# Performance work log

Hardware: AMD Instinct MI355X
Metric: run time of the kernel (lower is better)

Reference implementation:

```python
import jax, jax.numpy as jnp
import numpy as np

N = 50000      # nodes
E = 500000     # edges (avg degree 10)
IN = 256       # in_feats
HID = 64       # hid_feats (per-head out dim)
H = 4          # num_heads


def setup_inputs() -> dict:
    key = jax.random.key(0)
    ks = jax.random.split(key, 16)
    f32 = jnp.float32
    def rn(k, shape, s=0.05):
        return jax.random.normal(k, shape, dtype=f32) * s
    return {
        "x": jax.random.normal(ks[0], (N, IN), dtype=f32),
        "src": jax.random.randint(ks[1], (E,), 0, N, dtype=jnp.int32),
        "dst": jax.random.randint(ks[2], (E,), 0, N, dtype=jnp.int32),
        "embed_W": rn(ks[3], (IN, HID)), "embed_b": jnp.zeros((HID,), f32),
        "W1": rn(ks[4], (HID, H * HID)),
        "al1": rn(ks[5], (H, HID)), "ar1": rn(ks[6], (H, HID)),
        "b1": jnp.zeros((H * HID,), f32),
        "W2": rn(ks[7], (H * HID, H * HID)),
        "al2": rn(ks[8], (H, HID)), "ar2": rn(ks[9], (H, HID)),
        "b2": jnp.zeros((H * HID,), f32),
        "p1_W": rn(ks[10], (H * HID, HID)), "p1_b": jnp.zeros((HID,), f32),
        "p2_W": rn(ks[11], (HID, 1)), "p2_b": jnp.zeros((1,), f32),
    }


def _gat_conv(x, W, al, ar, b, src, dst):
    """DGL GATConv: linear proj, per-edge LeakyReLU attention, edge softmax over dst, scatter-sum."""
    feat = (x @ W).reshape(N, H, HID)                    # [N,H,F]
    el = jnp.einsum('nhf,hf->nh', feat, al)              # [N,H]
    er = jnp.einsum('nhf,hf->nh', feat, ar)              # [N,H]
    e = jax.nn.leaky_relu(el[src] + er[dst], 0.2)        # [E,H]
    m = jax.ops.segment_max(e, dst, num_segments=N)      # per-dst max (stable softmax)
    ex = jnp.exp(e - m[dst])                             # [E,H]
    s = jax.ops.segment_sum(ex, dst, num_segments=N)     # [N,H]
    alpha = ex / s[dst]                                  # edge softmax weights
    out = jax.ops.segment_sum(alpha[:, :, None] * feat[src], dst, num_segments=N)  # [N,H,F]
    return out + b.reshape(1, H, HID)


def reference(x, src, dst, embed_W, embed_b, W1, al1, ar1, b1,
              W2, al2, ar2, b2, p1_W, p1_b, p2_W, p2_b):
    h = x @ embed_W + embed_b                                        # embed: [N,HID]
    h = jax.nn.relu(_gat_conv(h, W1, al1, ar1, b1, src, dst))        # [N,H,HID]
    h = h.reshape(N, H * HID)
    h = jax.nn.relu(_gat_conv(h, W2, al2, ar2, b2, src, dst))        # [N,H,HID]
    h = h.reshape(N, H * HID)
    return jax.nn.sigmoid((h @ p1_W + p1_b) @ p2_W + p2_b)           # [N,1]
```

## Files before the change

### kernel.cpp

```cpp
#include <hip/hip_runtime.h>
#include <hip/hip_bf16.h>

#define NN 50000
#define NE 500000
#define C_HH 256

typedef __attribute__((ext_vector_type(8))) short s16x8;
typedef __attribute__((ext_vector_type(4))) float f32x4;
typedef __attribute__((ext_vector_type(4))) unsigned short u16x4;
typedef unsigned short ushort_t;

__device__ __forceinline__ float lrelu(float x) { return x > 0.f ? x : 0.2f * x; }

__device__ __forceinline__ ushort_t f2bf(float f) {
  unsigned u = __float_as_uint(f);
  u = (u + 0x7FFFu + ((u >> 16) & 1u)) >> 16;
  return (ushort_t)u;
}
__device__ __forceinline__ float bf2f(ushort_t u) {
  return __uint_as_float(((unsigned)u) << 16);
}
__device__ __forceinline__ float sel_head(float4 v, int head) {
  const float x0 = (head & 1) ? v.y : v.x;
  const float x1 = (head & 1) ? v.w : v.z;
  return (head & 2) ? x1 : x0;
}

__global__ __launch_bounds__(256) void prep_kernel(const float* __restrict__ eW,
                                                   const float* __restrict__ W1,
                                                   const float* __restrict__ eb,
                                                   const float* __restrict__ W2,
                                                   const float* __restrict__ p1W,
                                                   const float* __restrict__ p1b,
                                                   const float* __restrict__ p2W,
                                                   const float* __restrict__ p2b,
                                                   ushort_t* __restrict__ WcT,
                                                   ushort_t* __restrict__ w2T,
                                                   float* __restrict__ bc,
                                                   float* __restrict__ qv,
                                                   float* __restrict__ cv) {
  int idx = blockIdx.x * 256 + threadIdx.x;
  if (idx < 65536) {
    const int n = idx >> 8, k = idx & 255;
    float s = 0.f;
#pragma unroll 8
    for (int j = 0; j < 64; ++j) s = fmaf(eW[k * 64 + j], W1[j * 256 + n], s);
    WcT[idx] = f2bf(s);
  } else if (idx < 131072) {
    idx -= 65536;
    const int n = idx >> 8, k = idx & 255;
    w2T[idx] = f2bf(W2[k * 256 + n]);
  } else if (idx < 131328) {
    const int n = idx - 131072;
    float s = 0.f;
#pragma unroll 8
    for (int j = 0; j < 64; ++j) s = fmaf(eb[j], W1[j * 256 + n], s);
    bc[n] = s;
  } else if (idx < 131584) {
    const int k = idx - 131328;
    float s = 0.f;
#pragma unroll 8
    for (int j = 0; j < 64; ++j) s = fmaf(p1W[k * 64 + j], p2W[j], s);
    qv[k] = s;
  } else if (idx == 131584) {
    float s = p2b[0];
    for (int j = 0; j < 64; ++j) s = fmaf(p1b[j], p2W[j], s);
    cv[0] = s;
  }
}

template <bool A_F32, bool BIAS>
__global__ __launch_bounds__(256) void gemm_fused(const void* __restrict__ Ain,
                                                  const ushort_t* __restrict__ WT,
                                                  const float* __restrict__ bc,
                                                  const float* __restrict__ al,
                                                  const float* __restrict__ ar,
                                                  float* __restrict__ el,
                                                  float* __restrict__ er,
                                                  ushort_t* __restrict__ Cout, int M) {
  const int wid = threadIdx.x >> 6;
  const int lane = threadIdx.x & 63;
  const int row0 = blockIdx.x * 32;
  const int rA = lane & 15;
  const int kg = lane >> 4;
  const int c0 = wid * 64;

  f32x4 acc[2][4] = {};
  const s16x8 zf = {0, 0, 0, 0, 0, 0, 0, 0};
  const bool v0 = (row0 + rA) < M;
  const bool v1 = (row0 + 16 + rA) < M;
  const ushort_t* Wbase = WT + (size_t)(c0 + rA) * 256;

  for (int ks = 0; ks < 8; ++ks) {
    const int k0 = ks * 32 + kg * 8;
    s16x8 a0 = zf, a1 = zf;
    if (A_F32) {
      const float* Af = (const float*)Ain;
      if (v0) {
        const f32x4 u0 = *reinterpret_cast<const f32x4*>(Af + (size_t)(row0 + rA) * 256 + k0);
        const f32x4 u1 = *reinterpret_cast<const f32x4*>(Af + (size_t)(row0 + rA) * 256 + k0 + 4);
        a0[0] = (short)f2bf(u0[0]); a0[1] = (short)f2bf(u0[1]);
        a0[2] = (short)f2bf(u0[2]); a0[3] = (short)f2bf(u0[3]);
        a0[4] = (short)f2bf(u1[0]); a0[5] = (short)f2bf(u1[1]);
        a0[6] = (short)f2bf(u1[2]); a0[7] = (short)f2bf(u1[3]);
      }
      if (v1) {
        const f32x4 u0 = *reinterpret_cast<const f32x4*>(Af + (size_t)(row0 + 16 + rA) * 256 + k0);
        const f32x4 u1 = *reinterpret_cast<const f32x4*>(Af + (size_t)(row0 + 16 + rA) * 256 + k0 + 4);
        a1[0] = (short)f2bf(u0[0]); a1[1] = (short)f2bf(u0[1]);
        a1[2] = (short)f2bf(u0[2]); a1[3] = (short)f2bf(u0[3]);
        a1[4] = (short)f2bf(u1[0]); a1[5] = (short)f2bf(u1[1]);
        a1[6] = (short)f2bf(u1[2]); a1[7] = (short)f2bf(u1[3]);
      }
    } else {
      const ushort_t* Ab = (const ushort_t*)Ain;
      if (v0) a0 = *reinterpret_cast<const s16x8*>(Ab + (size_t)(row0 + rA) * 256 + k0);
      if (v1) a1 = *reinterpret_cast<const s16x8*>(Ab + (size_t)(row0 + 16 + rA) * 256 + k0);
    }
#pragma unroll
    for (int nt = 0; nt < 4; ++nt) {
      const s16x8 b = *reinterpret_cast<const s16x8*>(Wbase + nt * 16 * 256 + k0);
      acc[0][nt] = __builtin_amdgcn_mfma_f32_16x16x32_bf16(a0, b, acc[0][nt], 0, 0, 0);
      acc[1][nt] = __builtin_amdgcn_mfma_f32_16x16x32_bf16(a1, b, acc[1][nt], 0, 0, 0);
    }
  }

  if (BIAS) {
#pragma unroll
    for (int nt = 0; nt < 4; ++nt) {
      const float bv = bc[c0 + nt * 16 + rA];
#pragma unroll
      for (int mt = 0; mt < 2; ++mt)
#pragma unroll
        for (int i = 0; i < 4; ++i) acc[mt][nt][i] += bv;
    }
  }

#pragma unroll
  for (int nt = 0; nt < 4; ++nt) {
    const int col = c0 + nt * 16 + rA;
#pragma unroll
    for (int mt = 0; mt < 2; ++mt) {
#pragma unroll
      for (int i = 0; i < 4; ++i) {
        const int row = row0 + mt * 16 + kg * 4 + i;
        if (row < M) Cout[(size_t)row * 256 + col] = f2bf(acc[mt][nt][i]);
      }
    }
  }

  float alv[4], arv[4];
#pragma unroll
  for (int nt = 0; nt < 4; ++nt) {
    alv[nt] = al[c0 + nt * 16 + rA];
    arv[nt] = ar[c0 + nt * 16 + rA];
  }
#pragma unroll
  for (int mt = 0; mt < 2; ++mt) {
#pragma unroll
    for (int i = 0; i < 4; ++i) {
      float e = 0.f, r = 0.f;
#pragma unroll
      for (int nt = 0; nt < 4; ++nt) {
        e = fmaf(acc[mt][nt][i], alv[nt], e);
        r = fmaf(acc[mt][nt][i], arv[nt], r);
      }
#pragma unroll
      for (int m = 1; m < 16; m <<= 1) {
        e += __shfl_xor(e, m);
        r += __shfl_xor(r, m);
      }
      const int row = row0 + mt * 16 + kg * 4 + i;
      if (rA == 0 && row < M) {
        el[row * 4 + wid] = e;
        er[row * 4 + wid] = r;
      }
    }
  }
}

__global__ __launch_bounds__(256) void hist_kernel(const int* __restrict__ dst,
                                                   int* __restrict__ rowptr) {
  const int e = blockIdx.x * 256 + threadIdx.x;
  if (e < NE) atomicAdd(&rowptr[dst[e]], 1);
}

__global__ __launch_bounds__(256) void scan1_kernel(int* __restrict__ rowptr,
                                                    int* __restrict__ partial) {
  __shared__ int sh[256];
  const int t = threadIdx.x;
  const int i = blockIdx.x * 256 + t;
  const int v = (i < NN) ? rowptr[i] : 0;
  sh[t] = v;
  __syncthreads();
#pragma unroll
  for (int off = 1; off < 256; off <<= 1) {
    int x = (t >= off) ? sh[t - off] : 0;
    __syncthreads();
    sh[t] += x;
    __syncthreads();
  }
  if (i < NN) rowptr[i] = sh[t] - v;
  if (t == 255) partial[blockIdx.x] = sh[255];
}

__global__ __launch_bounds__(256) void scan2_kernel(int* __restrict__ partial, int npb) {
  __shared__ int sh[256];
  const int t = threadIdx.x;
  const int v = (t < npb) ? partial[t] : 0;
  sh[t] = v;
  __syncthreads();
#pragma unroll
  for (int off = 1; off < 256; off <<= 1) {
    int x = (t >= off) ? sh[t - off] : 0;
    __syncthreads();
    sh[t] += x;
    __syncthreads();
  }
  if (t < npb) partial[t] = sh[t] - v;
}

__global__ __launch_bounds__(256) void scan3_kernel(int* __restrict__ rowptr,
                                                    const int* __restrict__ partial,
                                                    int* __restrict__ cursor) {
  const int i = blockIdx.x * 256 + threadIdx.x;
  if (i < NN) {
    const int r = rowptr[i] + partial[i >> 8];
    rowptr[i] = r;
    cursor[i] = r;
  } else if (i == NN) {
    rowptr[NN] = NE;
  }
}

__global__ __launch_bounds__(256) void scatter_kernel(const int* __restrict__ src,
                                                      const int* __restrict__ dst,
                                                      int* __restrict__ cursor,
                                                      int* __restrict__ sorted_src) {
  const int e = blockIdx.x * 256 + threadIdx.x;
  if (e >= NE) return;
  const int pos = atomicAdd(&cursor[dst[e]], 1);
  sorted_src[pos] = src[e];
}

__global__ __launch_bounds__(256) void aggr_fused_kernel(const int* __restrict__ rowptr,
                                                         const int* __restrict__ sorted_src,
                                                         const float* __restrict__ el,
                                                         const float* __restrict__ er,
                                                         const ushort_t* __restrict__ featb,
                                                         const float* __restrict__ bias,
                                                         ushort_t* __restrict__ out) {
  const int node = blockIdx.x * 4 + (threadIdx.x >> 6);
  const int lane = threadIdx.x & 63;
  const int head = lane >> 4;
  const int start = rowptr[node];
  const int end = rowptr[node + 1];
  const float erh = sel_head(*reinterpret_cast<const float4*>(er + node * 4), head);
  const size_t lofs = (size_t)lane * 4;

  float a0 = 0.f, a1 = 0.f, a2 = 0.f, a3 = 0.f, s = 0.f;
  int e = start;
  const int end4 = end - 3;
  for (; e < end4; e += 4) {
    const int sn0 = sorted_src[e + 0];
    const int sn1 = sorted_src[e + 1];
    const int sn2 = sorted_src[e + 2];
    const int sn3 = sorted_src[e + 3];
    const float4 A0 = *reinterpret_cast<const float4*>(el + sn0 * 4);
    const float4 A1 = *reinterpret_cast<const float4*>(el + sn1 * 4);
    const float4 A2 = *reinterpret_cast<const float4*>(el + sn2 * 4);
    const float4 A3 = *reinterpret_cast<const float4*>(el + sn3 * 4);
    const u16x4 F0 = *reinterpret_cast<const u16x4*>(featb + (size_t)sn0 * C_HH + lofs);
    const u16x4 F1 = *reinterpret_cast<const u16x4*>(featb + (size_t)sn1 * C_HH + lofs);
    const u16x4 F2 = *reinterpret_cast<const u16x4*>(featb + (size_t)sn2 * C_HH + lofs);
    const u16x4 F3 = *reinterpret_cast<const u16x4*>(featb + (size_t)sn3 * C_HH + lofs);
    const float w0 = __expf(lrelu(sel_head(A0, head) + erh));
    const float w1 = __expf(lrelu(sel_head(A1, head) + erh));
    const float w2 = __expf(lrelu(sel_head(A2, head) + erh));
    const float w3 = __expf(lrelu(sel_head(A3, head) + erh));
    a0 = fmaf(w0, bf2f(F0[0]), a0); a1 = fmaf(w0, bf2f(F0[1]), a1);
    a2 = fmaf(w0, bf2f(F0[2]), a2); a3 = fmaf(w0, bf2f(F0[3]), a3);
    a0 = fmaf(w1, bf2f(F1[0]), a0); a1 = fmaf(w1, bf2f(F1[1]), a1);
    a2 = fmaf(w1, bf2f(F1[2]), a2); a3 = fmaf(w1, bf2f(F1[3]), a3);
    a0 = fmaf(w2, bf2f(F2[0]), a0); a1 = fmaf(w2, bf2f(F2[1]), a1);
    a2 = fmaf(w2, bf2f(F2[2]), a2); a3 = fmaf(w2, bf2f(F2[3]), a3);
    a0 = fmaf(w3, bf2f(F3[0]), a0); a1 = fmaf(w3, bf2f(F3[1]), a1);
    a2 = fmaf(w3, bf2f(F3[2]), a2); a3 = fmaf(w3, bf2f(F3[3]), a3);
    s += (w0 + w1) + (w2 + w3);
  }
  for (; e < end; ++e) {
    const int sn = sorted_src[e];
    const float4 A = *reinterpret_cast<const float4*>(el + sn * 4);
    const u16x4 F = *reinterpret_cast<const u16x4*>(featb + (size_t)sn * C_HH + lofs);
    const float w = __expf(lrelu(sel_head(A, head) + erh));
    a0 = fmaf(w, bf2f(F[0]), a0); a1 = fmaf(w, bf2f(F[1]), a1);
    a2 = fmaf(w, bf2f(F[2]), a2); a3 = fmaf(w, bf2f(F[3]), a3);
    s += w;
  }

  float r0 = 0.f, r1 = 0.f, r2 = 0.f, r3 = 0.f;
  if (end > start) {
    const float inv = 1.f / s;
    r0 = a0 * inv; r1 = a1 * inv; r2 = a2 * inv; r3 = a3 * inv;
  }
  const float4 bb = *reinterpret_cast<const float4*>(bias + lane * 4);
  u16x4 o;
  o[0] = f2bf(fmaxf(r0 + bb.x, 0.f));
  o[1] = f2bf(fmaxf(r1 + bb.y, 0.f));
  o[2] = f2bf(fmaxf(r2 + bb.z, 0.f));
  o[3] = f2bf(fmaxf(r3 + bb.w, 0.f));
  *reinterpret_cast<u16x4*>(out + (size_t)node * C_HH + lane * 4) = o;
}

__global__ __launch_bounds__(256) void head_kernel(const ushort_t* __restrict__ houtb,
                                                   const float* __restrict__ qv,
                                                   const float* __restrict__ cv,
                                                   float* __restrict__ out) {
  const int node = blockIdx.x * 4 + (threadIdx.x >> 6);
  const int lane = threadIdx.x & 63;
  const u16x4 f = *reinterpret_cast<const u16x4*>(houtb + (size_t)node * C_HH + lane * 4);
  const float4 q = *reinterpret_cast<const float4*>(qv + lane * 4);
  float v = bf2f(f[0]) * q.x + bf2f(f[1]) * q.y + bf2f(f[2]) * q.z + bf2f(f[3]) * q.w;
#pragma unroll
  for (int off = 32; off; off >>= 1) v += __shfl_xor(v, off);
  if (lane == 0) out[node] = 1.f / (1.f + __expf(-(v + cv[0])));
}

extern "C" void kernel_launch(void* const* d_in, const int* in_sizes, int n_in,
                              void* d_out, int out_size, void* d_ws, size_t ws_size,
                              hipStream_t stream) {
  const float* x = (const float*)d_in[0];
  const int* src = (const int*)d_in[1];
  const int* dst = (const int*)d_in[2];
  const float* embed_W = (const float*)d_in[3];
  const float* embed_b = (const float*)d_in[4];
  const float* W1 = (const float*)d_in[5];
  const float* al1 = (const float*)d_in[6];
  const float* ar1 = (const float*)d_in[7];
  const float* b1 = (const float*)d_in[8];
  const float* W2 = (const float*)d_in[9];
  const float* al2 = (const float*)d_in[10];
  const float* ar2 = (const float*)d_in[11];
  const float* b2 = (const float*)d_in[12];
  const float* p1_W = (const float*)d_in[13];
  const float* p1_b = (const float*)d_in[14];
  const float* p2_W = (const float*)d_in[15];
  const float* p2_b = (const float*)d_in[16];

  char* ws = (char*)d_ws;
  ushort_t* featb = (ushort_t*)(ws + 0);
  ushort_t* houtb = (ushort_t*)(ws + 25600000);
  float* el = (float*)(ws + 51200000);
  float* er = (float*)(ws + 52000000);
  int* rowptr = (int*)(ws + 52800000);
  int* cursor = (int*)(ws + 53100000);
  int* partial = (int*)(ws + 53400000);
  int* sorted_src = (int*)(ws + 53500000);
  ushort_t* WcT = (ushort_t*)(ws + 55600000);
  ushort_t* w2T = (ushort_t*)(ws + 55800000);
  float* bc = (float*)(ws + 56000000);
  float* qv = (float*)(ws + 56010000);
  float* cv = (float*)(ws + 56020000);

  const int gEdge = (NE + 255) / 256;
  const int nScanB = (NN + 255) / 256;
  const int gGemm = (NN + 31) / 32;
  const int gNode = NN / 4;

  hipMemsetAsync(rowptr, 0, (NN + 1) * sizeof(int), stream);
  hist_kernel<<<gEdge, 256, 0, stream>>>(dst, rowptr);
  scan1_kernel<<<nScanB, 256, 0, stream>>>(rowptr, partial);
  scan2_kernel<<<1, 256, 0, stream>>>(partial, nScanB);
  scan3_kernel<<<nScanB + 1, 256, 0, stream>>>(rowptr, partial, cursor);
  scatter_kernel<<<gEdge, 256, 0, stream>>>(src, dst, cursor, sorted_src);

  prep_kernel<<<515, 256, 0, stream>>>(embed_W, W1, embed_b, W2, p1_W, p1_b, p2_W, p2_b,
                                       WcT, w2T, bc, qv, cv);

  gemm_fused<true, true><<<gGemm, 256, 0, stream>>>(x, WcT, bc, al1, ar1, el, er, featb, NN);
  aggr_fused_kernel<<<gNode, 256, 0, stream>>>(rowptr, sorted_src, el, er, featb, b1, houtb);

  gemm_fused<false, false><<<gGemm, 256, 0, stream>>>(houtb, w2T, nullptr, al2, ar2, el, er, featb, NN);
  aggr_fused_kernel<<<gNode, 256, 0, stream>>>(rowptr, sorted_src, el, er, featb, b2, houtb);

  head_kernel<<<gNode, 256, 0, stream>>>(houtb, qv, cv, (float*)d_out);
}
```

Measured before the change: 379.2 us.

## Fuse output head into second aggregation, preload GEMM operands, unroll edges by 8

The second GAT aggregation now computes the projection-head dot product and sigmoid directly, instead of writing bf16 hidden features for a separate head kernel. That removes one launch and a full write and re-read of the node features. The GEMM now issues all A and B loads up front into registers before the MFMA loop, with launch bounds asking for 2 blocks per SM. This raises register pressure in exchange for more memory-level parallelism. The aggregation edge loop is unrolled to 8 gathers per iteration to keep more loads in flight.

```diff
diff --git a/kernel.cpp b/kernel.cpp
--- a/kernel.cpp
+++ b/kernel.cpp
@@ -70,14 +70,14 @@
 }
 
 template <bool A_F32, bool BIAS>
-__global__ __launch_bounds__(256) void gemm_fused(const void* __restrict__ Ain,
-                                                  const ushort_t* __restrict__ WT,
-                                                  const float* __restrict__ bc,
-                                                  const float* __restrict__ al,
-                                                  const float* __restrict__ ar,
-                                                  float* __restrict__ el,
-                                                  float* __restrict__ er,
-                                                  ushort_t* __restrict__ Cout, int M) {
+__global__ __launch_bounds__(256, 2) void gemm_fused(const void* __restrict__ Ain,
+                                                     const ushort_t* __restrict__ WT,
+                                                     const float* __restrict__ bc,
+                                                     const float* __restrict__ al,
+                                                     const float* __restrict__ ar,
+                                                     float* __restrict__ el,
+                                                     float* __restrict__ er,
+                                                     ushort_t* __restrict__ Cout, int M) {
   const int wid = threadIdx.x >> 6;
   const int lane = threadIdx.x & 63;
   const int row0 = blockIdx.x * 32;
@@ -85,43 +85,65 @@
   const int kg = lane >> 4;
   const int c0 = wid * 64;
 
-  f32x4 acc[2][4] = {};
   const s16x8 zf = {0, 0, 0, 0, 0, 0, 0, 0};
   const bool v0 = (row0 + rA) < M;
   const bool v1 = (row0 + 16 + rA) < M;
   const ushort_t* Wbase = WT + (size_t)(c0 + rA) * 256;
 
+  s16x8 a0[8], a1[8];
+  if (A_F32) {
+    const float* Af = (const float*)Ain;
+    const float* Ar0 = Af + (size_t)(row0 + rA) * 256;
+    const float* Ar1 = Af + (size_t)(row0 + 16 + rA) * 256;
+    const f32x4 zf4 = {0.f, 0.f, 0.f, 0.f};
+    f32x4 af0[8][2], af1[8][2];
+#pragma unroll
+    for (int ks = 0; ks < 8; ++ks) {
+      const int k0 = ks * 32 + kg * 8;
+      af0[ks][0] = v0 ? *reinterpret_cast<const f32x4*>(Ar0 + k0) : zf4;
+      af0[ks][1] = v0 ? *reinterpret_cast<const f32x4*>(Ar0 + k0 + 4) : zf4;
+      af1[ks][0] = v1 ? *reinterpret_cast<const f32x4*>(Ar1 + k0) : zf4;
+      af1[ks][1] = v1 ? *reinterpret_cast<const f32x4*>(Ar1 + k0 + 4) : zf4;
+    }
+#pragma unroll
+    for (int ks = 0; ks < 8; ++ks) {
+#pragma unroll
+      for (int h = 0; h < 2; ++h) {
+#pragma unroll
+        for (int j = 0; j < 4; ++j) {
+          a0[ks][h * 4 + j] = (short)f2bf(af0[ks][h][j]);
+          a1[ks][h * 4 + j] = (short)f2bf(af1[ks][h][j]);
+        }
+      }
+    }
+  } else {
+    const ushort_t* Ab = (const ushort_t*)Ain;
+    const ushort_t* Ar0 = Ab + (size_t)(row0 + rA) * 256;
+    const ushort_t* Ar1 = Ab + (size_t)(row0 + 16 + rA) * 256;
+#pragma unroll
+    for (int ks = 0; ks < 8; ++ks) {
+      const int k0 = ks * 32 + kg * 8;
+      a0[ks] = v0 ? *reinterpret_cast<const s16x8*>(Ar0 + k0) : zf;
+      a1[ks] = v1 ? *reinterpret_cast<const s16x8*>(Ar1 + k0) : zf;
+    }
+  }
+
+  s16x8 b[8][4];
+#pragma unroll
   for (int ks = 0; ks < 8; ++ks) {
     const int k0 = ks * 32 + kg * 8;
-    s16x8 a0 = zf, a1 = zf;
-    if (A_F32) {
-      const float* Af = (const float*)Ain;
-      if (v0) {
-        const f32x4 u0 = *reinterpret_cast<const f32x4*>(Af + (size_t)(row0 + rA) * 256 + k0);
-        const f32x4 u1 = *reinterpret_cast<const f32x4*>(Af + (size_t)(row0 + rA) * 256 + k0 + 4);
-        a0[0] = (short)f2bf(u0[0]); a0[1] = (short)f2bf(u0[1]);
-        a0[2] = (short)f2bf(u0[2]); a0[3] = (short)f2bf(u0[3]);
-        a0[4] = (short)f2bf(u1[0]); a0[5] = (short)f2bf(u1[1]);
-        a0[6] = (short)f2bf(u1[2]); a0[7] = (short)f2bf(u1[3]);
-      }
-      if (v1) {
-        const f32x4 u0 = *reinterpret_cast<const f32x4*>(Af + (size_t)(row0 + 16 + rA) * 256 + k0);
-        const f32x4 u1 = *reinterpret_cast<const f32x4*>(Af + (size_t)(row0 + 16 + rA) * 256 + k0 + 4);
-        a1[0] = (short)f2bf(u0[0]); a1[1] = (short)f2bf(u0[1]);
-        a1[2] = (short)f2bf(u0[2]); a1[3] = (short)f2bf(u0[3]);
-        a1[4] = (short)f2bf(u1[0]); a1[5] = (short)f2bf(u1[1]);
-        a1[6] = (short)f2bf(u1[2]); a1[7] = (short)f2bf(u1[3]);
-      }
-    } else {
-      const ushort_t* Ab = (const ushort_t*)Ain;
-      if (v0) a0 = *reinterpret_cast<const s16x8*>(Ab + (size_t)(row0 + rA) * 256 + k0);
-      if (v1) a1 = *reinterpret_cast<const s16x8*>(Ab + (size_t)(row0 + 16 + rA) * 256 + k0);
-    }
+#pragma unroll
+    for (int nt = 0; nt < 4; ++nt)
+      b[ks][nt] = *reinterpret_cast<const s16x8*>(Wbase + nt * 16 * 256 + k0);
+  }
+
+  f32x4 acc[2][4] = {};
+#pragma unroll
+  for (int ks = 0; ks < 8; ++ks) {
 #pragma unroll
     for (int nt = 0; nt < 4; ++nt) {
-      const s16x8 b = *reinterpret_cast<const s16x8*>(Wbase + nt * 16 * 256 + k0);
-      acc[0][nt] = __builtin_amdgcn_mfma_f32_16x16x32_bf16(a0, b, acc[0][nt], 0, 0, 0);
-      acc[1][nt] = __builtin_amdgcn_mfma_f32_16x16x32_bf16(a1, b, acc[1][nt], 0, 0, 0);
+      acc[0][nt] = __builtin_amdgcn_mfma_f32_16x16x32_bf16(a0[ks], b[ks][nt], acc[0][nt], 0, 0, 0);
+      acc[1][nt] = __builtin_amdgcn_mfma_f32_16x16x32_bf16(a1[ks], b[ks][nt], acc[1][nt], 0, 0, 0);
     }
   }
 
@@ -243,13 +265,27 @@
   sorted_src[pos] = src[e];
 }
 
+#define EDGE_BODY(SN, AV, FV)                                    \
+  {                                                              \
+    const float w_ = __expf(lrelu(sel_head(AV, head) + erh));    \
+    a0 = fmaf(w_, bf2f(FV[0]), a0);                              \
+    a1 = fmaf(w_, bf2f(FV[1]), a1);                              \
+    a2 = fmaf(w_, bf2f(FV[2]), a2);                              \
+    a3 = fmaf(w_, bf2f(FV[3]), a3);                              \
+    s += w_;                                                     \
+  }
+
+template <bool HEAD>
 __global__ __launch_bounds__(256) void aggr_fused_kernel(const int* __restrict__ rowptr,
                                                          const int* __restrict__ sorted_src,
                                                          const float* __restrict__ el,
                                                          const float* __restrict__ er,
                                                          const ushort_t* __restrict__ featb,
                                                          const float* __restrict__ bias,
-                                                         ushort_t* __restrict__ out) {
+                                                         ushort_t* __restrict__ out,
+                                                         const float* __restrict__ qv,
+                                                         const float* __restrict__ cv,
+                                                         float* __restrict__ outf) {
   const int node = blockIdx.x * 4 + (threadIdx.x >> 6);
   const int lane = threadIdx.x & 63;
   const int head = lane >> 4;
@@ -260,8 +296,37 @@
 
   float a0 = 0.f, a1 = 0.f, a2 = 0.f, a3 = 0.f, s = 0.f;
   int e = start;
-  const int end4 = end - 3;
-  for (; e < end4; e += 4) {
+  for (; e + 8 <= end; e += 8) {
+    const int sn0 = sorted_src[e + 0];
+    const int sn1 = sorted_src[e + 1];
+    const int sn2 = sorted_src[e + 2];
+    const int sn3 = sorted_src[e + 3];
+    const int sn4 = sorted_src[e + 4];
+    const int sn5 = sorted_src[e + 5];
+    const int sn6 = sorted_src[e + 6];
+    const int sn7 = sorted_src[e + 7];
+    const float4 A0 = *reinterpret_cast<const float4*>(el + sn0 * 4);
+    const float4 A1 = *reinterpret_cast<const float4*>(el + sn1 * 4);
+    const float4 A2 = *reinterpret_cast<const float4*>(el + sn2 * 4);
+    const float4 A3 = *reinterpret_cast<const float4*>(el + sn3 * 4);
+    const float4 A4 = *reinterpret_cast<const float4*>(el + sn4 * 4);
+    const float4 A5 = *reinterpret_cast<const float4*>(el + sn5 * 4);
+    const float4 A6 = *reinterpret_cast<const float4*>(el + sn6 * 4);
+    const float4 A7 = *reinterpret_cast<const float4*>(el + sn7 * 4);
+    const u16x4 F0 = *reinterpret_cast<const u16x4*>(featb + (size_t)sn0 * C_HH + lofs);
+    const u16x4 F1 = *reinterpret_cast<const u16x4*>(featb + (size_t)sn1 * C_HH + lofs);
+    const u16x4 F2 = *reinterpret_cast<const u16x4*>(featb + (size_t)sn2 * C_HH + lofs);
+    const u16x4 F3 = *reinterpret_cast<const u16x4*>(featb + (size_t)sn3 * C_HH + lofs);
+    const u16x4 F4 = *reinterpret_cast<const u16x4*>(featb + (size_t)sn4 * C_HH + lofs);
+    const u16x4 F5 = *reinterpret_cast<const u16x4*>(featb + (size_t)sn5 * C_HH + lofs);
+    const u16x4 F6 = *reinterpret_cast<const u16x4*>(featb + (size_t)sn6 * C_HH + lofs);
+    const u16x4 F7 = *reinterpret_cast<const u16x4*>(featb + (size_t)sn7 * C_HH + lofs);
+    EDGE_BODY(sn0, A0, F0) EDGE_BODY(sn1, A1, F1)
+    EDGE_BODY(sn2, A2, F2) EDGE_BODY(sn3, A3, F3)
+    EDGE_BODY(sn4, A4, F4) EDGE_BODY(sn5, A5, F5)
+    EDGE_BODY(sn6, A6, F6) EDGE_BODY(sn7, A7, F7)
+  }
+  if (e + 4 <= end) {
     const int sn0 = sorted_src[e + 0];
     const int sn1 = sorted_src[e + 1];
     const int sn2 = sorted_src[e + 2];
@@ -274,28 +339,15 @@
     const u16x4 F1 = *reinterpret_cast<const u16x4*>(featb + (size_t)sn1 * C_HH + lofs);
     const u16x4 F2 = *reinterpret_cast<const u16x4*>(featb + (size_t)sn2 * C_HH + lofs);
     const u16x4 F3 = *reinterpret_cast<const u16x4*>(featb + (size_t)sn3 * C_HH + lofs);
-    const float w0 = __expf(lrelu(sel_head(A0, head) + erh));
-    const float w1 = __expf(lrelu(sel_head(A1, head) + erh));
-    const float w2 = __expf(lrelu(sel_head(A2, head) + erh));
-    const float w3 = __expf(lrelu(sel_head(A3, head) + erh));
-    a0 = fmaf(w0, bf2f(F0[0]), a0); a1 = fmaf(w0, bf2f(F0[1]), a1);
-    a2 = fmaf(w0, bf2f(F0[2]), a2); a3 = fmaf(w0, bf2f(F0[3]), a3);
-    a0 = fmaf(w1, bf2f(F1[0]), a0); a1 = fmaf(w1, bf2f(F1[1]), a1);
-    a2 = fmaf(w1, bf2f(F1[2]), a2); a3 = fmaf(w1, bf2f(F1[3]), a3);
-    a0 = fmaf(w2, bf2f(F2[0]), a0); a1 = fmaf(w2, bf2f(F2[1]), a1);
-    a2 = fmaf(w2, bf2f(F2[2]), a2); a3 = fmaf(w2, bf2f(F2[3]), a3);
-    a0 = fmaf(w3, bf2f(F3[0]), a0); a1 = fmaf(w3, bf2f(F3[1]), a1);
-    a2 = fmaf(w3, bf2f(F3[2]), a2); a3 = fmaf(w3, bf2f(F3[3]), a3);
-    s += (w0 + w1) + (w2 + w3);
+    EDGE_BODY(sn0, A0, F0) EDGE_BODY(sn1, A1, F1)
+    EDGE_BODY(sn2, A2, F2) EDGE_BODY(sn3, A3, F3)
+    e += 4;
   }
   for (; e < end; ++e) {
     const int sn = sorted_src[e];
     const float4 A = *reinterpret_cast<const float4*>(el + sn * 4);
     const u16x4 F = *reinterpret_cast<const u16x4*>(featb + (size_t)sn * C_HH + lofs);
-    const float w = __expf(lrelu(sel_head(A, head) + erh));
-    a0 = fmaf(w, bf2f(F[0]), a0); a1 = fmaf(w, bf2f(F[1]), a1);
-    a2 = fmaf(w, bf2f(F[2]), a2); a3 = fmaf(w, bf2f(F[3]), a3);
-    s += w;
+    EDGE_BODY(sn, A, F)
   }
 
   float r0 = 0.f, r1 = 0.f, r2 = 0.f, r3 = 0.f;
@@ -304,26 +356,22 @@
     r0 = a0 * inv; r1 = a1 * inv; r2 = a2 * inv; r3 = a3 * inv;
   }
   const float4 bb = *reinterpret_cast<const float4*>(bias + lane * 4);
-  u16x4 o;
-  o[0] = f2bf(fmaxf(r0 + bb.x, 0.f));
-  o[1] = f2bf(fmaxf(r1 + bb.y, 0.f));
-  o[2] = f2bf(fmaxf(r2 + bb.z, 0.f));
-  o[3] = f2bf(fmaxf(r3 + bb.w, 0.f));
-  *reinterpret_cast<u16x4*>(out + (size_t)node * C_HH + lane * 4) = o;
-}
-
-__global__ __launch_bounds__(256) void head_kernel(const ushort_t* __restrict__ houtb,
-                                                   const float* __restrict__ qv,
-                                                   const float* __restrict__ cv,
-                                                   float* __restrict__ out) {
-  const int node = blockIdx.x * 4 + (threadIdx.x >> 6);
-  const int lane = threadIdx.x & 63;
-  const u16x4 f = *reinterpret_cast<const u16x4*>(houtb + (size_t)node * C_HH + lane * 4);
-  const float4 q = *reinterpret_cast<const float4*>(qv + lane * 4);
-  float v = bf2f(f[0]) * q.x + bf2f(f[1]) * q.y + bf2f(f[2]) * q.z + bf2f(f[3]) * q.w;
-#pragma unroll
-  for (int off = 32; off; off >>= 1) v += __shfl_xor(v, off);
-  if (lane == 0) out[node] = 1.f / (1.f + __expf(-(v + cv[0])));
+  r0 = fmaxf(r0 + bb.x, 0.f);
+  r1 = fmaxf(r1 + bb.y, 0.f);
+  r2 = fmaxf(r2 + bb.z, 0.f);
+  r3 = fmaxf(r3 + bb.w, 0.f);
+
+  if (!HEAD) {
+    u16x4 o;
+    o[0] = f2bf(r0); o[1] = f2bf(r1); o[2] = f2bf(r2); o[3] = f2bf(r3);
+    *reinterpret_cast<u16x4*>(out + (size_t)node * C_HH + lofs) = o;
+  } else {
+    const float4 q = *reinterpret_cast<const float4*>(qv + lane * 4);
+    float v = fmaf(r0, q.x, fmaf(r1, q.y, fmaf(r2, q.z, r3 * q.w)));
+#pragma unroll
+    for (int off = 32; off; off >>= 1) v += __shfl_xor(v, off);
+    if (lane == 0) outf[node] = 1.f / (1.f + __expf(-(v + cv[0])));
+  }
 }
 
 extern "C" void kernel_launch(void* const* d_in, const int* in_sizes, int n_in,
@@ -378,10 +426,11 @@
                                        WcT, w2T, bc, qv, cv);
 
   gemm_fused<true, true><<<gGemm, 256, 0, stream>>>(x, WcT, bc, al1, ar1, el, er, featb, NN);
-  aggr_fused_kernel<<<gNode, 256, 0, stream>>>(rowptr, sorted_src, el, er, featb, b1, houtb);
-
-  gemm_fused<false, false><<<gGemm, 256, 0, stream>>>(houtb, w2T, nullptr, al2, ar2, el, er, featb, NN);
-  aggr_fused_kernel<<<gNode, 256, 0, stream>>>(rowptr, sorted_src, el, er, featb, b2, houtb);
-
-  head_kernel<<<gNode, 256, 0, stream>>>(houtb, qv, cv, (float*)d_out);
-}
+  aggr_fused_kernel<false><<<gNode, 256, 0, stream>>>(rowptr, sorted_src, el, er, featb, b1,
+                                                      houtb, nullptr, nullptr, nullptr);
+
+  gemm_fused<false, false><<<gGemm, 256, 0, stream>>>(houtb, w2T, nullptr, al2, ar2, el, er,
+                                                      featb, NN);
+  aggr_fused_kernel<true><<<gNode, 256, 0, stream>>>(rowptr, sorted_src, el, er, featb, b2,
+                                                     nullptr, qv, cv, (float*)d_out);
+}
```

Result: slower. 389.3 us (+2.7%).
